# Kernel optimization log

Hardware: AMD Instinct MI355X
Metric: run time of the kernel (lower is better)

The kernel has to match this reference:

```python
import jax, jax.numpy as jnp
import numpy as np

B, N, C, K = 2, 20000, 256, 16
H = C // 2  # gate hidden

def _ln(x, g, b, eps=1e-5):
    m = jnp.mean(x, axis=-1, keepdims=True)
    v = jnp.mean((x - m) ** 2, axis=-1, keepdims=True)
    return (x - m) * jax.lax.rsqrt(v + eps) * g + b

def setup_inputs() -> dict:
    key = jax.random.key(0)
    ks = jax.random.split(key, 16)
    s = 0.02
    return {
        'x_l0': jax.random.normal(ks[0], (B, N, C), jnp.float32),
        'x_l1': jax.random.normal(ks[1], (B, N, C), jnp.float32),
        'x_l2': jax.random.normal(ks[2], (B, N, C), jnp.float32),
        'x_l3': jax.random.normal(ks[3], (B, N, C), jnp.float32),
        'knn_idx': jax.random.randint(ks[4], (N, K), 0, N, jnp.int32),
        'Wq': jax.random.normal(ks[5], (3, C, C), jnp.float32) * s,
        'bq': jnp.zeros((3, C), jnp.float32),
        'Wk': jax.random.normal(ks[6], (3, C, C), jnp.float32) * s,
        'bk': jnp.zeros((3, C), jnp.float32),
        'Wv': jax.random.normal(ks[7], (3, C, C), jnp.float32) * s,
        'bv': jnp.zeros((3, C), jnp.float32),
        'ln_g': jnp.ones((3, C), jnp.float32),
        'ln_b': jnp.zeros((3, C), jnp.float32),
        'Wg1': jax.random.normal(ks[8], (H, C), jnp.float32) * s,
        'bg1': jnp.zeros((H,), jnp.float32),
        'Wg2': jax.random.normal(ks[9], (3, H), jnp.float32) * s,
        'bg2': jnp.zeros((3,), jnp.float32),
        'fn_g': jnp.ones((C,), jnp.float32),
        'fn_b': jnp.zeros((C,), jnp.float32),
    }

def reference(x_l0, x_l1, x_l2, x_l3, knn_idx, Wq, bq, Wk, bk, Wv, bv,
              ln_g, ln_b, Wg1, bg1, Wg2, bg2, fn_g, fn_b):
    c = x_l3.shape[-1]
    scale = 1.0 / jnp.sqrt(jnp.asarray(c, x_l3.dtype))

    def block(xq, i):
        Q = xq @ Wq[i].T + bq[i]            # (B,N,C)
        Kf = x_l3 @ Wk[i].T + bk[i]         # (B,N,C)
        Vf = x_l3 @ Wv[i].T + bv[i]
        Kk = Kf[:, knn_idx]                 # (B,N,K,C) gather along node dim
        Vk = Vf[:, knn_idx]
        s = jnp.einsum('bnc,bnkc->bnk', Q, Kk) * scale
        a = jax.nn.softmax(s, axis=-1)
        o = jnp.einsum('bnk,bnkc->bnc', a, Vk)
        return _ln(o + Q, ln_g[i], ln_b[i])

    Os = [block(x, i) for i, x in enumerate((x_l0, x_l1, x_l2))]
    h = jax.nn.relu(x_l3 @ Wg1.T + bg1)
    alpha = jax.nn.softmax(h @ Wg2.T + bg2, axis=-1)  # (B,N,3)
    out = sum(alpha[..., i:i + 1] * Os[i] for i in range(3))
    return _ln(out + x_l3, fn_g, fn_b)
```

## Files before the change

kernel.cpp:

```cpp
#include <hip/hip_runtime.h>

#define B_ 2
#define N_ 20000
#define C_ 256
#define K_ 16
#define H_ 128
#define ROWS (B_ * N_)
#define MT 313
#define MPAD (MT * 128)

typedef __attribute__((ext_vector_type(8))) short bf16x8;
typedef __attribute__((ext_vector_type(4))) float f32x4;

__device__ __forceinline__ float us2f(unsigned short u) {
    return __uint_as_float(((unsigned int)u) << 16);
}
__device__ __forceinline__ unsigned short f2us(float f) {
    unsigned int u = __float_as_uint(f);
    unsigned int r = (u + 0x7fffu + ((u >> 16) & 1u)) >> 16;
    return (unsigned short)r;
}
__device__ __forceinline__ float wred(float v) {
#pragma unroll
    for (int off = 32; off > 0; off >>= 1) v += __shfl_xor(v, off, 64);
    return v;
}
__device__ __forceinline__ void gld_lds16(const unsigned short* g, unsigned short* l) {
    __builtin_amdgcn_global_load_lds(
        (__attribute__((address_space(1))) void*)(g),
        (__attribute__((address_space(3))) void*)(l), 16, 0, 0);
}

extern "C" __global__ void __launch_bounds__(256)
cvtx_kernel(const float* __restrict__ x3, const float* __restrict__ x0,
            const float* __restrict__ x1, const float* __restrict__ x2,
            unsigned short* __restrict__ d3, unsigned short* __restrict__ dq, int n4) {
    const int y = blockIdx.y;
    const float* src = (y == 0) ? x3 : (y == 1 ? x0 : (y == 2 ? x1 : x2));
    unsigned short* dst = (y == 0) ? d3 : (dq + (size_t)(y - 1) * MPAD * C_);
    int t = blockIdx.x * 256 + threadIdx.x;
    if (t >= n4) return;
    float4 v = ((const float4*)src)[t];
    ushort4 o;
    o.x = f2us(v.x); o.y = f2us(v.y); o.z = f2us(v.z); o.w = f2us(v.w);
    ((ushort4*)dst)[t] = o;
}

extern "C" __global__ void __launch_bounds__(256)
cvtw_kernel(const float* __restrict__ s0, const float* __restrict__ s1,
            const float* __restrict__ s2, const float* __restrict__ s3,
            unsigned short* __restrict__ d0, unsigned short* __restrict__ d1,
            unsigned short* __restrict__ d2, unsigned short* __restrict__ d3) {
    const int y = blockIdx.y;
    const float* src = (y == 0) ? s0 : (y == 1 ? s1 : (y == 2 ? s2 : s3));
    unsigned short* dst = (y == 0) ? d0 : (y == 1 ? d1 : (y == 2 ? d2 : d3));
    const int n4 = (y < 3) ? (3 * C_ * C_ / 4) : (H_ * C_ / 4);
    int t = blockIdx.x * 256 + threadIdx.x;
    if (t >= n4) return;
    float4 v = ((const float4*)src)[t];
    ushort4 o;
    o.x = f2us(v.x); o.y = f2us(v.y); o.z = f2us(v.z); o.w = f2us(v.w);
    ((ushort4*)dst)[t] = o;
}

__device__ __forceinline__ void gemm_tile_body(
    const unsigned short* __restrict__ A, const unsigned short* __restrict__ W,
    const float* __restrict__ bias, unsigned short* __restrict__ O,
    const int m0, const int n0, const int ldo) {
    const int tid = threadIdx.x;
    const int w = tid >> 6, lane = tid & 63;
    const int l15 = lane & 15, l4 = lane >> 4;
    const int rowq = (w >> 1) * 64;
    const int colq = (w & 1) * 64;

    __shared__ unsigned short As[128 * 64];
    __shared__ unsigned short Bs[128 * 64];

    f32x4 acc[4][4] = {};

    const int srow = w * 8 + (lane >> 3);
    const int schunk = lane & 7;

    for (int k0 = 0; k0 < 256; k0 += 64) {
        __syncthreads();
#pragma unroll
        for (int issue = 0; issue < 4; ++issue) {
            const int lrow = issue * 32 + srow;
            const int sc = (schunk ^ ((lrow >> 1) & 7)) * 8;
            gld_lds16(A + (size_t)(m0 + lrow) * 256 + k0 + sc, As + issue * 2048 + w * 512);
            gld_lds16(W + (size_t)(n0 + lrow) * 256 + k0 + sc, Bs + issue * 2048 + w * 512);
        }
        __syncthreads();
#pragma unroll
        for (int ks = 0; ks < 2; ++ks) {
            bf16x8 a[4], b[4];
#pragma unroll
            for (int i = 0; i < 4; ++i) {
                const int ra = rowq + i * 16 + l15;
                const int ch = ((ks << 2) | l4) ^ ((ra >> 1) & 7);
                a[i] = *(const bf16x8*)&As[ra * 64 + ch * 8];
            }
#pragma unroll
            for (int j = 0; j < 4; ++j) {
                const int rb = colq + j * 16 + l15;
                const int ch = ((ks << 2) | l4) ^ ((rb >> 1) & 7);
                b[j] = *(const bf16x8*)&Bs[rb * 64 + ch * 8];
            }
#pragma unroll
            for (int i = 0; i < 4; ++i)
#pragma unroll
                for (int j = 0; j < 4; ++j)
                    acc[i][j] = __builtin_amdgcn_mfma_f32_16x16x32_bf16(b[j], a[i], acc[i][j], 0, 0, 0);
        }
    }

#pragma unroll
    for (int i = 0; i < 4; ++i) {
        const int grow = m0 + rowq + i * 16 + l15;
        if (grow < ROWS) {
#pragma unroll
            for (int j = 0; j < 4; ++j) {
                const int gcol = n0 + colq + j * 16 + l4 * 4;
                const float4 b4 = *(const float4*)&bias[gcol];
                uint2 pk;
                pk.x = (unsigned int)f2us(acc[i][j][0] + b4.x) |
                       ((unsigned int)f2us(acc[i][j][1] + b4.y) << 16);
                pk.y = (unsigned int)f2us(acc[i][j][2] + b4.z) |
                       ((unsigned int)f2us(acc[i][j][3] + b4.w) << 16);
                *(uint2*)&O[(size_t)grow * ldo + gcol] = pk;
            }
        }
    }
}

extern "C" __global__ void __launch_bounds__(256)
gemm_kv(const unsigned short* __restrict__ x3bf,
        const unsigned short* __restrict__ wk, const unsigned short* __restrict__ wv,
        const float* __restrict__ bk, const float* __restrict__ bv,
        unsigned short* __restrict__ kv) {
    const int panel = blockIdx.x;
    const int zi = panel >> 1;
    const int i = zi >> 1;
    const int isV = zi & 1;
    const unsigned short* W = (isV ? wv : wk) + (size_t)i * C_ * C_;
    const float* bias = (isV ? bv : bk) + i * C_;
    unsigned short* O = kv + (size_t)zi * MPAD * C_;
    gemm_tile_body(x3bf, W, bias, O, blockIdx.y * 128, (panel & 1) * 128, C_);
}

extern "C" __global__ void __launch_bounds__(256)
gemm_h(const unsigned short* __restrict__ x3bf, const unsigned short* __restrict__ wg1,
       const float* __restrict__ bg1, unsigned short* __restrict__ Hout) {
    gemm_tile_body(x3bf, wg1, bg1, Hout, blockIdx.x * 128, 0, H_);
}

extern "C" __global__ void __launch_bounds__(256)
gemm_q(const unsigned short* __restrict__ A, const unsigned short* __restrict__ W,
       const float* __restrict__ bias, unsigned short* __restrict__ O) {
    gemm_tile_body(A, W, bias, O, blockIdx.x * 128, blockIdx.y * 128, C_);
}

extern "C" __global__ void __launch_bounds__(256)
gate2_kernel(const unsigned short* __restrict__ Hbf, const float* __restrict__ Wg2,
             const float* __restrict__ bg2, float* __restrict__ alpha) {
    const int tid = threadIdx.x;
    const int w = tid >> 6, lane = tid & 63;
    const int row = blockIdx.x * 4 + w;
    const float h0 = fmaxf(us2f(Hbf[(size_t)row * H_ + lane]), 0.f);
    const float h1 = fmaxf(us2f(Hbf[(size_t)row * H_ + 64 + lane]), 0.f);
    float lg[3];
#pragma unroll
    for (int l = 0; l < 3; ++l) {
        const float* w2 = Wg2 + l * H_;
        lg[l] = wred(h0 * w2[lane] + h1 * w2[lane + 64]) + bg2[l];
    }
    float m = fmaxf(lg[0], fmaxf(lg[1], lg[2]));
    float e0 = expf(lg[0] - m), e1 = expf(lg[1] - m), e2 = expf(lg[2] - m);
    float inv = 1.f / (e0 + e1 + e2);
    if (lane == 0) {
        alpha[row * 3 + 0] = e0 * inv;
        alpha[row * 3 + 1] = e1 * inv;
        alpha[row * 3 + 2] = e2 * inv;
    }
}

__device__ __forceinline__ void attn_core(
    const unsigned short* __restrict__ q, const unsigned short* __restrict__ kf,
    const unsigned short* __restrict__ vf, const int* __restrict__ knn,
    const int row, const int b, const int n, const int t,
    float* __restrict__ qv, float* __restrict__ o) {
    const unsigned short* qp = q + (size_t)row * C_ + t * 4;
#pragma unroll
    for (int j = 0; j < 4; ++j) {
        ushort4 u = *(const ushort4*)(qp + j * 64);
        qv[j * 4 + 0] = us2f(u.x);
        qv[j * 4 + 1] = us2f(u.y);
        qv[j * 4 + 2] = us2f(u.z);
        qv[j * 4 + 3] = us2f(u.w);
    }

    int idxs[K_];
    float s[K_];
#pragma unroll
    for (int k = 0; k < K_; ++k) {
        idxs[k] = knn[n * K_ + k];
        const unsigned short* kp = kf + ((size_t)b * N_ + idxs[k]) * C_ + t * 4;
        float p = 0.f;
#pragma unroll
        for (int j = 0; j < 4; ++j) {
            ushort4 u = *(const ushort4*)(kp + j * 64);
            p += qv[j * 4 + 0] * us2f(u.x) + qv[j * 4 + 1] * us2f(u.y) +
                 qv[j * 4 + 2] * us2f(u.z) + qv[j * 4 + 3] * us2f(u.w);
        }
#pragma unroll
        for (int off = 1; off < 16; off <<= 1) p += __shfl_xor(p, off, 64);
        s[k] = p * 0.0625f;
    }

    float m = s[0];
#pragma unroll
    for (int k = 1; k < K_; ++k) m = fmaxf(m, s[k]);
    float sum = 0.f;
#pragma unroll
    for (int k = 0; k < K_; ++k) {
        s[k] = __expf(s[k] - m);
        sum += s[k];
    }
    const float inv = 1.f / sum;

#pragma unroll
    for (int c = 0; c < 16; ++c) o[c] = 0.f;
#pragma unroll
    for (int k = 0; k < K_; ++k) {
        const float a = s[k] * inv;
        const unsigned short* vp = vf + ((size_t)b * N_ + idxs[k]) * C_ + t * 4;
#pragma unroll
        for (int j = 0; j < 4; ++j) {
            ushort4 u = *(const ushort4*)(vp + j * 64);
            o[j * 4 + 0] += a * us2f(u.x);
            o[j * 4 + 1] += a * us2f(u.y);
            o[j * 4 + 2] += a * us2f(u.z);
            o[j * 4 + 3] += a * us2f(u.w);
        }
    }
}

extern "C" __global__ void __launch_bounds__(256)
attn_kernel(const unsigned short* __restrict__ q, const unsigned short* __restrict__ kf,
            const unsigned short* __restrict__ vf, const int* __restrict__ knn,
            const float* __restrict__ alpha, const float* __restrict__ lng,
            const float* __restrict__ lnb, float* __restrict__ accum, const int iblk) {
    const int tid = threadIdx.x;
    const int t = tid & 15;
    const int row = blockIdx.x * 16 + (tid >> 4);
    const int b = row / N_;
    const int n = row - b * N_;
    float qv[16], o[16];
    attn_core(q, kf, vf, knn, row, b, n, t, qv, o);

    float s1 = 0.f, s2 = 0.f;
#pragma unroll
    for (int c = 0; c < 16; ++c) {
        o[c] += qv[c];
        s1 += o[c];
        s2 += o[c] * o[c];
    }
#pragma unroll
    for (int off = 1; off < 16; off <<= 1) {
        s1 += __shfl_xor(s1, off, 64);
        s2 += __shfl_xor(s2, off, 64);
    }
    const float mean = s1 * (1.f / C_);
    const float var = s2 * (1.f / C_) - mean * mean;
    const float rstd = rsqrtf(var + 1e-5f);

    const float a = alpha[row * 3 + iblk];
    const float* gp = lng + iblk * C_ + t * 4;
    const float* bp = lnb + iblk * C_ + t * 4;
    float* ap = accum + (size_t)row * C_ + t * 4;
#pragma unroll
    for (int j = 0; j < 4; ++j) {
        float4 gg = *(const float4*)(gp + j * 64);
        float4 bb = *(const float4*)(bp + j * 64);
        float4 y;
        y.x = ((o[j * 4 + 0] - mean) * rstd * gg.x + bb.x) * a;
        y.y = ((o[j * 4 + 1] - mean) * rstd * gg.y + bb.y) * a;
        y.z = ((o[j * 4 + 2] - mean) * rstd * gg.z + bb.z) * a;
        y.w = ((o[j * 4 + 3] - mean) * rstd * gg.w + bb.w) * a;
        if (iblk == 0) {
            *(float4*)(ap + j * 64) = y;
        } else {
            float4 p = *(const float4*)(ap + j * 64);
            p.x += y.x; p.y += y.y; p.z += y.z; p.w += y.w;
            *(float4*)(ap + j * 64) = p;
        }
    }
}

extern "C" __global__ void __launch_bounds__(256)
attn_last(const unsigned short* __restrict__ q, const unsigned short* __restrict__ kf,
          const unsigned short* __restrict__ vf, const int* __restrict__ knn,
          const float* __restrict__ alpha, const float* __restrict__ lng,
          const float* __restrict__ lnb, const float* __restrict__ accum,
          const float* __restrict__ x3, const float* __restrict__ fng,
          const float* __restrict__ fnb, float* __restrict__ out) {
    const int tid = threadIdx.x;
    const int t = tid & 15;
    const int row = blockIdx.x * 16 + (tid >> 4);
    const int b = row / N_;
    const int n = row - b * N_;
    float qv[16], o[16];
    attn_core(q, kf, vf, knn, row, b, n, t, qv, o);

    float s1 = 0.f, s2 = 0.f;
#pragma unroll
    for (int c = 0; c < 16; ++c) {
        o[c] += qv[c];
        s1 += o[c];
        s2 += o[c] * o[c];
    }
#pragma unroll
    for (int off = 1; off < 16; off <<= 1) {
        s1 += __shfl_xor(s1, off, 64);
        s2 += __shfl_xor(s2, off, 64);
    }
    const float mean = s1 * (1.f / C_);
    const float var = s2 * (1.f / C_) - mean * mean;
    const float rstd = rsqrtf(var + 1e-5f);

    const float a = alpha[row * 3 + 2];
    const float* gp = lng + 2 * C_ + t * 4;
    const float* bp = lnb + 2 * C_ + t * 4;
    const float* ap = accum + (size_t)row * C_ + t * 4;
    const float* xp = x3 + (size_t)row * C_ + t * 4;
    float u1 = 0.f, u2 = 0.f;
#pragma unroll
    for (int j = 0; j < 4; ++j) {
        float4 gg = *(const float4*)(gp + j * 64);
        float4 bb = *(const float4*)(bp + j * 64);
        float4 pa = *(const float4*)(ap + j * 64);
        float4 xv = *(const float4*)(xp + j * 64);
        o[j * 4 + 0] = pa.x + xv.x + ((o[j * 4 + 0] - mean) * rstd * gg.x + bb.x) * a;
        o[j * 4 + 1] = pa.y + xv.y + ((o[j * 4 + 1] - mean) * rstd * gg.y + bb.y) * a;
        o[j * 4 + 2] = pa.z + xv.z + ((o[j * 4 + 2] - mean) * rstd * gg.z + bb.z) * a;
        o[j * 4 + 3] = pa.w + xv.w + ((o[j * 4 + 3] - mean) * rstd * gg.w + bb.w) * a;
    }
#pragma unroll
    for (int c = 0; c < 16; ++c) {
        u1 += o[c];
        u2 += o[c] * o[c];
    }
#pragma unroll
    for (int off = 1; off < 16; off <<= 1) {
        u1 += __shfl_xor(u1, off, 64);
        u2 += __shfl_xor(u2, off, 64);
    }
    const float fmean = u1 * (1.f / C_);
    const float fvar = u2 * (1.f / C_) - fmean * fmean;
    const float frstd = rsqrtf(fvar + 1e-5f);

    const float* fgp = fng + t * 4;
    const float* fbp = fnb + t * 4;
    float* op = out + (size_t)row * C_ + t * 4;
#pragma unroll
    for (int j = 0; j < 4; ++j) {
        float4 gg = *(const float4*)(fgp + j * 64);
        float4 bb = *(const float4*)(fbp + j * 64);
        float4 y;
        y.x = (o[j * 4 + 0] - fmean) * frstd * gg.x + bb.x;
        y.y = (o[j * 4 + 1] - fmean) * frstd * gg.y + bb.y;
        y.z = (o[j * 4 + 2] - fmean) * frstd * gg.z + bb.z;
        y.w = (o[j * 4 + 3] - fmean) * frstd * gg.w + bb.w;
        *(float4*)(op + j * 64) = y;
    }
}

extern "C" void kernel_launch(void* const* d_in, const int* in_sizes, int n_in,
                              void* d_out, int out_size, void* d_ws, size_t ws_size,
                              hipStream_t stream) {
    const float* x0 = (const float*)d_in[0];
    const float* x1 = (const float*)d_in[1];
    const float* x2 = (const float*)d_in[2];
    const float* x3 = (const float*)d_in[3];
    const int* knn = (const int*)d_in[4];
    const float* Wq = (const float*)d_in[5];
    const float* bq = (const float*)d_in[6];
    const float* Wk = (const float*)d_in[7];
    const float* bk = (const float*)d_in[8];
    const float* Wv = (const float*)d_in[9];
    const float* bv = (const float*)d_in[10];
    const float* ln_g = (const float*)d_in[11];
    const float* ln_b = (const float*)d_in[12];
    const float* Wg1 = (const float*)d_in[13];
    const float* bg1 = (const float*)d_in[14];
    const float* Wg2 = (const float*)d_in[15];
    const float* bg2 = (const float*)d_in[16];
    const float* fn_g = (const float*)d_in[17];
    const float* fn_b = (const float*)d_in[18];
    float* out = (float*)d_out;

    unsigned char* w8 = (unsigned char*)d_ws;
    const size_t XBF = (size_t)MPAD * C_ * 2;
    const size_t HBF = (size_t)MPAD * H_ * 2;
    const size_t WBLOB = (size_t)3 * C_ * C_ * 2;
    const size_t WG1B = (size_t)H_ * C_ * 2;
    const size_t XE = (size_t)MPAD * C_;

    unsigned short* x3bf  = (unsigned short*)(w8);
    unsigned short* xqall = (unsigned short*)(w8 + XBF);
    unsigned short* qbf   = (unsigned short*)(w8 + 4 * XBF);
    unsigned short* kvbf  = (unsigned short*)(w8 + 5 * XBF);
    unsigned short* Hbf   = (unsigned short*)(w8 + 11 * XBF);
    unsigned short* wqbf  = (unsigned short*)(w8 + 11 * XBF + HBF);
    unsigned short* wkbf  = (unsigned short*)(w8 + 11 * XBF + HBF + WBLOB);
    unsigned short* wvbf  = (unsigned short*)(w8 + 11 * XBF + HBF + 2 * WBLOB);
    unsigned short* wg1bf = (unsigned short*)(w8 + 11 * XBF + HBF + 3 * WBLOB);
    float* alpha = (float*)(w8 + 11 * XBF + HBF + 3 * WBLOB + WG1B);

    const int xn4 = ROWS * C_ / 4;
    const int wn4 = 3 * C_ * C_ / 4;

    cvtx_kernel<<<dim3((xn4 + 255) / 256, 4), 256, 0, stream>>>(
        x3, x0, x1, x2, x3bf, xqall, xn4);
    cvtw_kernel<<<dim3((wn4 + 255) / 256, 4), 256, 0, stream>>>(
        Wq, Wk, Wv, Wg1, wqbf, wkbf, wvbf, wg1bf);

    gemm_h<<<dim3(MT), 256, 0, stream>>>(x3bf, wg1bf, bg1, Hbf);
    gate2_kernel<<<ROWS / 4, 256, 0, stream>>>(Hbf, Wg2, bg2, alpha);

    gemm_kv<<<dim3(12, MT), 256, 0, stream>>>(x3bf, wkbf, wvbf, bk, bv, kvbf);

    for (int i = 0; i < 3; ++i) {
        gemm_q<<<dim3(MT, 2), 256, 0, stream>>>(
            xqall + (size_t)i * XE, wqbf + (size_t)i * C_ * C_, bq + i * C_, qbf);
        const unsigned short* kf = kvbf + (size_t)(2 * i) * XE;
        const unsigned short* vf = kvbf + (size_t)(2 * i + 1) * XE;
        if (i < 2) {
            attn_kernel<<<ROWS / 16, 256, 0, stream>>>(qbf, kf, vf, knn, alpha,
                                                       ln_g, ln_b, out, i);
        } else {
            attn_last<<<ROWS / 16, 256, 0, stream>>>(qbf, kf, vf, knn, alpha,
                                                     ln_g, ln_b, out, x3,
                                                     fn_g, fn_b, out);
        }
    }
}
```

Before: 627.6 us.

## Fuse fp32-to-bf16 conversion of query inputs into Q GEMM and interleave per-block KV GEMMs

The separate bf16 conversion pass over x_l0..x_l2 is removed. The Q GEMM now reads fp32 activations directly, converts them in registers and writes them into swizzled LDS, while B still uses global_load_lds. The single large K/V GEMM over all three blocks is split into one per block, launched just before that block's attention and reusing one K/V buffer, which cuts workspace size and may keep K/V warm in cache for the gather. The cost is that A loads are no longer async-to-LDS and fp32 A traffic is twice as wide inside the GEMM, and there are more, smaller launches.

```diff
diff --git a/kernel.cpp b/kernel.cpp
--- a/kernel.cpp
+++ b/kernel.cpp
@@ -32,12 +32,7 @@
 }
 
 extern "C" __global__ void __launch_bounds__(256)
-cvtx_kernel(const float* __restrict__ x3, const float* __restrict__ x0,
-            const float* __restrict__ x1, const float* __restrict__ x2,
-            unsigned short* __restrict__ d3, unsigned short* __restrict__ dq, int n4) {
-    const int y = blockIdx.y;
-    const float* src = (y == 0) ? x3 : (y == 1 ? x0 : (y == 2 ? x1 : x2));
-    unsigned short* dst = (y == 0) ? d3 : (dq + (size_t)(y - 1) * MPAD * C_);
+cvt_kernel(const float* __restrict__ src, unsigned short* __restrict__ dst, int n4) {
     int t = blockIdx.x * 256 + threadIdx.x;
     if (t >= n4) return;
     float4 v = ((const float4*)src)[t];
@@ -133,31 +128,115 @@
     }
 }
 
-extern "C" __global__ void __launch_bounds__(256)
-gemm_kv(const unsigned short* __restrict__ x3bf,
-        const unsigned short* __restrict__ wk, const unsigned short* __restrict__ wv,
-        const float* __restrict__ bk, const float* __restrict__ bv,
-        unsigned short* __restrict__ kv) {
+__device__ __forceinline__ void gemm_tile_body_f32a(
+    const float* __restrict__ A, const unsigned short* __restrict__ W,
+    const float* __restrict__ bias, unsigned short* __restrict__ O,
+    const int m0, const int n0, const int ldo) {
+    const int tid = threadIdx.x;
+    const int w = tid >> 6, lane = tid & 63;
+    const int l15 = lane & 15, l4 = lane >> 4;
+    const int rowq = (w >> 1) * 64;
+    const int colq = (w & 1) * 64;
+
+    __shared__ unsigned short As[128 * 64];
+    __shared__ unsigned short Bs[128 * 64];
+
+    f32x4 acc[4][4] = {};
+
+    const int srow = w * 8 + (lane >> 3);
+    const int schunk = lane & 7;
+    const int arow = tid >> 4;
+    const int ac4 = (tid & 15) * 4;
+
+    for (int k0 = 0; k0 < 256; k0 += 64) {
+        float4 f4[8];
+#pragma unroll
+        for (int issue = 0; issue < 8; ++issue) {
+            const int lrow = issue * 16 + arow;
+            f4[issue] = *(const float4*)&A[(size_t)(m0 + lrow) * 256 + k0 + ac4];
+        }
+        __syncthreads();
+#pragma unroll
+        for (int issue = 0; issue < 4; ++issue) {
+            const int lrow = issue * 32 + srow;
+            const int sc = (schunk ^ ((lrow >> 1) & 7)) * 8;
+            gld_lds16(W + (size_t)(n0 + lrow) * 256 + k0 + sc, Bs + issue * 2048 + w * 512);
+        }
+#pragma unroll
+        for (int issue = 0; issue < 8; ++issue) {
+            const int lrow = issue * 16 + arow;
+            const int off = lrow * 64 + (((ac4 >> 3) ^ ((lrow >> 1) & 7)) << 3) + (ac4 & 7);
+            uint2 pk;
+            pk.x = (unsigned int)f2us(f4[issue].x) | ((unsigned int)f2us(f4[issue].y) << 16);
+            pk.y = (unsigned int)f2us(f4[issue].z) | ((unsigned int)f2us(f4[issue].w) << 16);
+            *(uint2*)&As[off] = pk;
+        }
+        __syncthreads();
+#pragma unroll
+        for (int ks = 0; ks < 2; ++ks) {
+            bf16x8 a[4], b[4];
+#pragma unroll
+            for (int i = 0; i < 4; ++i) {
+                const int ra = rowq + i * 16 + l15;
+                const int ch = ((ks << 2) | l4) ^ ((ra >> 1) & 7);
+                a[i] = *(const bf16x8*)&As[ra * 64 + ch * 8];
+            }
+#pragma unroll
+            for (int j = 0; j < 4; ++j) {
+                const int rb = colq + j * 16 + l15;
+                const int ch = ((ks << 2) | l4) ^ ((rb >> 1) & 7);
+                b[j] = *(const bf16x8*)&Bs[rb * 64 + ch * 8];
+            }
+#pragma unroll
+            for (int i = 0; i < 4; ++i)
+#pragma unroll
+                for (int j = 0; j < 4; ++j)
+                    acc[i][j] = __builtin_amdgcn_mfma_f32_16x16x32_bf16(b[j], a[i], acc[i][j], 0, 0, 0);
+        }
+    }
+
+#pragma unroll
+    for (int i = 0; i < 4; ++i) {
+        const int grow = m0 + rowq + i * 16 + l15;
+        if (grow < ROWS) {
+#pragma unroll
+            for (int j = 0; j < 4; ++j) {
+                const int gcol = n0 + colq + j * 16 + l4 * 4;
+                const float4 b4 = *(const float4*)&bias[gcol];
+                uint2 pk;
+                pk.x = (unsigned int)f2us(acc[i][j][0] + b4.x) |
+                       ((unsigned int)f2us(acc[i][j][1] + b4.y) << 16);
+                pk.y = (unsigned int)f2us(acc[i][j][2] + b4.z) |
+                       ((unsigned int)f2us(acc[i][j][3] + b4.w) << 16);
+                *(uint2*)&O[(size_t)grow * ldo + gcol] = pk;
+            }
+        }
+    }
+}
+
+extern "C" __global__ void __launch_bounds__(256)
+gemm_kvi(const unsigned short* __restrict__ x3bf,
+         const unsigned short* __restrict__ wk, const unsigned short* __restrict__ wv,
+         const float* __restrict__ bk, const float* __restrict__ bv,
+         unsigned short* __restrict__ kv) {
     const int panel = blockIdx.x;
     const int zi = panel >> 1;
-    const int i = zi >> 1;
-    const int isV = zi & 1;
-    const unsigned short* W = (isV ? wv : wk) + (size_t)i * C_ * C_;
-    const float* bias = (isV ? bv : bk) + i * C_;
+    const unsigned short* W = zi ? wv : wk;
+    const float* bias = zi ? bv : bk;
     unsigned short* O = kv + (size_t)zi * MPAD * C_;
     gemm_tile_body(x3bf, W, bias, O, blockIdx.y * 128, (panel & 1) * 128, C_);
+}
+
+extern "C" __global__ void __launch_bounds__(256)
+gemm_q32(const float* __restrict__ xq, const unsigned short* __restrict__ wq,
+         const float* __restrict__ bq, unsigned short* __restrict__ O) {
+    gemm_tile_body_f32a(xq, wq, bq, O, blockIdx.y * 128, blockIdx.x * 128, C_);
 }
 
 extern "C" __global__ void __launch_bounds__(256)
 gemm_h(const unsigned short* __restrict__ x3bf, const unsigned short* __restrict__ wg1,
        const float* __restrict__ bg1, unsigned short* __restrict__ Hout) {
     gemm_tile_body(x3bf, wg1, bg1, Hout, blockIdx.x * 128, 0, H_);
-}
-
-extern "C" __global__ void __launch_bounds__(256)
-gemm_q(const unsigned short* __restrict__ A, const unsigned short* __restrict__ W,
-       const float* __restrict__ bias, unsigned short* __restrict__ O) {
-    gemm_tile_body(A, W, bias, O, blockIdx.x * 128, blockIdx.y * 128, C_);
 }
 
 extern "C" __global__ void __launch_bounds__(256)
@@ -407,40 +486,38 @@
     const size_t XE = (size_t)MPAD * C_;
 
     unsigned short* x3bf  = (unsigned short*)(w8);
-    unsigned short* xqall = (unsigned short*)(w8 + XBF);
-    unsigned short* qbf   = (unsigned short*)(w8 + 4 * XBF);
-    unsigned short* kvbf  = (unsigned short*)(w8 + 5 * XBF);
-    unsigned short* Hbf   = (unsigned short*)(w8 + 11 * XBF);
-    unsigned short* wqbf  = (unsigned short*)(w8 + 11 * XBF + HBF);
-    unsigned short* wkbf  = (unsigned short*)(w8 + 11 * XBF + HBF + WBLOB);
-    unsigned short* wvbf  = (unsigned short*)(w8 + 11 * XBF + HBF + 2 * WBLOB);
-    unsigned short* wg1bf = (unsigned short*)(w8 + 11 * XBF + HBF + 3 * WBLOB);
-    float* alpha = (float*)(w8 + 11 * XBF + HBF + 3 * WBLOB + WG1B);
+    unsigned short* qbf   = (unsigned short*)(w8 + XBF);
+    unsigned short* kvbf  = (unsigned short*)(w8 + 2 * XBF);
+    unsigned short* Hbf   = (unsigned short*)(w8 + 4 * XBF);
+    unsigned short* wqbf  = (unsigned short*)(w8 + 4 * XBF + HBF);
+    unsigned short* wkbf  = (unsigned short*)(w8 + 4 * XBF + HBF + WBLOB);
+    unsigned short* wvbf  = (unsigned short*)(w8 + 4 * XBF + HBF + 2 * WBLOB);
+    unsigned short* wg1bf = (unsigned short*)(w8 + 4 * XBF + HBF + 3 * WBLOB);
+    float* alpha = (float*)(w8 + 4 * XBF + HBF + 3 * WBLOB + WG1B);
 
     const int xn4 = ROWS * C_ / 4;
     const int wn4 = 3 * C_ * C_ / 4;
-
-    cvtx_kernel<<<dim3((xn4 + 255) / 256, 4), 256, 0, stream>>>(
-        x3, x0, x1, x2, x3bf, xqall, xn4);
+    const float* xq[3] = {x0, x1, x2};
+
+    cvt_kernel<<<(xn4 + 255) / 256, 256, 0, stream>>>(x3, x3bf, xn4);
     cvtw_kernel<<<dim3((wn4 + 255) / 256, 4), 256, 0, stream>>>(
         Wq, Wk, Wv, Wg1, wqbf, wkbf, wvbf, wg1bf);
 
     gemm_h<<<dim3(MT), 256, 0, stream>>>(x3bf, wg1bf, bg1, Hbf);
     gate2_kernel<<<ROWS / 4, 256, 0, stream>>>(Hbf, Wg2, bg2, alpha);
 
-    gemm_kv<<<dim3(12, MT), 256, 0, stream>>>(x3bf, wkbf, wvbf, bk, bv, kvbf);
-
     for (int i = 0; i < 3; ++i) {
-        gemm_q<<<dim3(MT, 2), 256, 0, stream>>>(
-            xqall + (size_t)i * XE, wqbf + (size_t)i * C_ * C_, bq + i * C_, qbf);
-        const unsigned short* kf = kvbf + (size_t)(2 * i) * XE;
-        const unsigned short* vf = kvbf + (size_t)(2 * i + 1) * XE;
+        gemm_kvi<<<dim3(4, MT), 256, 0, stream>>>(
+            x3bf, wkbf + (size_t)i * C_ * C_, wvbf + (size_t)i * C_ * C_,
+            bk + i * C_, bv + i * C_, kvbf);
+        gemm_q32<<<dim3(2, MT), 256, 0, stream>>>(
+            xq[i], wqbf + (size_t)i * C_ * C_, bq + i * C_, qbf);
         if (i < 2) {
-            attn_kernel<<<ROWS / 16, 256, 0, stream>>>(qbf, kf, vf, knn, alpha,
-                                                       ln_g, ln_b, out, i);
+            attn_kernel<<<ROWS / 16, 256, 0, stream>>>(qbf, kvbf, kvbf + XE, knn,
+                                                       alpha, ln_g, ln_b, out, i);
         } else {
-            attn_last<<<ROWS / 16, 256, 0, stream>>>(qbf, kf, vf, knn, alpha,
-                                                     ln_g, ln_b, out, x3,
+            attn_last<<<ROWS / 16, 256, 0, stream>>>(qbf, kvbf, kvbf + XE, knn,
+                                                     alpha, ln_g, ln_b, out, x3,
                                                      fn_g, fn_b, out);
         }
     }
```

New measurement: 623.0 us. About the same (-0.7%).
